# Performance work log

Measured on AMD Instinct MI355X. Metric: run time of the kernel, lower is better.

Reference implementation:

```python
import jax, jax.numpy as jnp
import numpy as np

GAMMA = 0.99
NUM_CODEWORDS = 512
CODEBOOK_DIM = 64


def setup_inputs() -> dict:
    key = jax.random.key(0)
    kx, kc = jax.random.split(key)
    x = jax.random.normal(kx, (32, 64, 64, 64), dtype=jnp.float32)  # [N,C,H,W]
    codebook = jax.random.normal(kc, (NUM_CODEWORDS, CODEBOOK_DIM), dtype=jnp.float32) / 2
    N_state = jnp.ones((NUM_CODEWORDS,), dtype=jnp.float32)
    m_state = codebook.copy()
    return {"x": x, "codebook": codebook, "N_state": N_state, "m_state": m_state}


def reference(x, codebook, N_state, m_state):
    N, C, H, W = x.shape
    K = codebook.shape[0]
    # flatten to tokens: [N*H*W, C]
    xf = jnp.transpose(x, (0, 2, 3, 1)).reshape(-1, C)
    d2 = (jnp.sum(xf * xf, axis=-1, keepdims=True)
          - 2.0 * (xf @ codebook.T)
          + jnp.sum(codebook * codebook, axis=-1)[None, :])
    index = jnp.argmin(d2, axis=1)  # [T]
    q = codebook[index].reshape(N, H, W, C).transpose(0, 3, 1, 2)  # [N,C,H,W]
    # straight-through estimator
    out = x + jax.lax.stop_gradient(q - x)
    # EMA update (training path, no_grad in original)
    counts = jax.ops.segment_sum(jnp.ones_like(index, dtype=x.dtype), index, num_segments=K)
    sums = jax.ops.segment_sum(xf, index, num_segments=K)  # [K,C]
    occupied = counts > 0
    N_new = jnp.where(occupied, N_state * GAMMA + counts * (1.0 - GAMMA), N_state)
    m_new = jnp.where(occupied[:, None], m_state * GAMMA + sums * (1.0 - GAMMA), m_state)
    codebook_new = m_new / N_new[:, None]
    return out, codebook_new, N_new, m_new
```

## Files before the change

### kernel.cpp

```cpp
#include <hip/hip_runtime.h>

static constexpr int Nn_ = 32, Cc_ = 64, Hh_ = 64, Ww_ = 64;
static constexpr int K_ = 512;
static constexpr int HW_ = Hh_ * Ww_;
static constexpr int CHW_ = Cc_ * HW_;
static constexpr int T_ = Nn_ * Hh_ * Ww_;
static constexpr int OUT_ELEMS = Nn_ * Cc_ * Hh_ * Ww_;
static constexpr int OFF_CB = OUT_ELEMS;
static constexpr int OFF_N  = OUT_ELEMS + 32768;
static constexpr int OFF_M  = OUT_ELEMS + 32768 + 512;

static constexpr int WS_IDX     = 0;
static constexpr int WS_FIXCNT  = T_;
static constexpr int WS_FIXLIST = T_ + 1;
static constexpr int WS_CBH     = 262148;
static constexpr int WS_CBL     = WS_CBH + 16384;
static constexpr int WS_CN      = WS_CBL + 16384;
static constexpr int WS_CNA     = WS_CN + 512;
static constexpr int WS_PART    = 295940;
static constexpr int SLICE_F    = K_ * Cc_ + K_;

static constexpr float THETA = 0.002f;

typedef _Float16 half8  __attribute__((ext_vector_type(8)));
typedef float    f32x16 __attribute__((ext_vector_type(16)));

__global__ __launch_bounds__(256) void k_prep(const float* __restrict__ cb,
                                              float* __restrict__ ws) {
    int j = blockIdx.x * 256 + threadIdx.x;
    if (j == 0) ((int*)(ws + WS_FIXCNT))[0] = 0;
    float v = cb[j];
    _Float16 h = (_Float16)v;
    _Float16 lo = (_Float16)(v - (float)h);
    ((_Float16*)(ws + WS_CBH))[j] = h;
    ((_Float16*)(ws + WS_CBL))[j] = lo;
    float sq = v * v;
#pragma unroll
    for (int m = 1; m < 64; m <<= 1) sq += __shfl_xor(sq, m);
    if ((threadIdx.x & 63) == 0) {
        int k = j >> 6;
        ws[WS_CN + k] = sq;
        int t = k >> 5, r5 = k & 31;
        int hi = (r5 >> 2) & 1;
        int reg = (r5 & 3) + 4 * (r5 >> 3);
        ws[WS_CNA + hi * 256 + t * 16 + reg] = sq;
    }
}

__global__ __launch_bounds__(256, 3) void k_assign(const float* __restrict__ x,
                                                   const float* __restrict__ cb,
                                                   float* __restrict__ ws,
                                                   float* __restrict__ out) {
    __shared__ alignas(16) unsigned char smem[52224];
    int* bi_s   = (int*)(smem + 51200);
    int* cert_s = (int*)(smem + 51712);

    const int b    = blockIdx.x;
    const int tid  = threadIdx.x;
    const int lane = tid & 63;
    const int wv   = tid >> 6;
    const int row0 = 2 * b, row1 = 2 * b + 1;
    const int xb0 = (row0 >> 6) * CHW_ + (row0 & 63) * Ww_;
    const int xb1 = (row1 >> 6) * CHW_ + (row1 & 63) * Ww_;

    {
        const int s  = tid & 31;
        const int c8 = tid >> 5;
        const int r  = s >> 4, wq = s & 15;
        half8 hp[4], lp[4];
#pragma unroll
        for (int stp = 0; stp < 8; ++stp) {
            int ch = c8 * 8 + stp;
            float4 v = *(const float4*)(x + (r ? xb1 : xb0) + ch * HW_ + 4 * wq);
            float vv[4] = {v.x, v.y, v.z, v.w};
#pragma unroll
            for (int j = 0; j < 4; ++j) {
                _Float16 h = (_Float16)vv[j];
                _Float16 lo = (_Float16)(vv[j] - (float)h);
                hp[j][stp] = h; lp[j][stp] = lo;
            }
        }
        const int blk = c8 ^ (wq & 7);
#pragma unroll
        for (int j = 0; j < 4; ++j) {
            int tt = 64 * r + 4 * wq + j;
            *(half8*)(smem + tt * 128 + blk * 16) = hp[j];
            *(half8*)(smem + 16384 + tt * 128 + blk * 16) = lp[j];
        }
        ((float*)(smem + 49152))[tid]       = ws[WS_CNA + tid];
        ((float*)(smem + 49152))[tid + 256] = ws[WS_CNA + tid + 256];
    }

    const char* cbh_g = (const char*)(ws + WS_CBH);
    const char* cbl_g = (const char*)(ws + WS_CBL);
    {
        float4 h4 = *(const float4*)(cbh_g + tid * 16);
        float4 l4 = *(const float4*)(cbl_g + tid * 16);
        int r = tid >> 3, p = (tid & 7) ^ (r & 7);
        *(float4*)(smem + 32768 + r * 128 + p * 16) = h4;
        *(float4*)(smem + 32768 + 4096 + r * 128 + p * 16) = l4;
    }
    __syncthreads();

    const int tb = 32 * wv + (lane & 31);
    const int hi = lane >> 5;
    half8 bh[4], bl[4];
    {
        const int tsw = (tb >> 2) & 7;
#pragma unroll
        for (int ks = 0; ks < 4; ++ks) {
            int blk = (2 * ks + hi) ^ tsw;
            bh[ks] = *(const half8*)(smem + tb * 128 + blk * 16);
            bl[ks] = *(const half8*)(smem + 16384 + tb * 128 + blk * 16);
        }
    }

    const float* cnA = (const float*)(smem + 49152);
    const int R = lane & 31;
    float bd1 = __int_as_float(0x7f800000);
    float bd2 = __int_as_float(0x7f800000);
    int bk1 = 0;

#pragma unroll 1
    for (int t = 0; t < 16; ++t) {
        const int cur = t & 1;
        float4 nh, nl;
        if (t < 15) {
            nh = *(const float4*)(cbh_g + (t + 1) * 4096 + tid * 16);
            nl = *(const float4*)(cbl_g + (t + 1) * 4096 + tid * 16);
        }
        const char* cb_b = (const char*)smem + 32768 + cur * 8192;
        half8 ah[4], al[4];
#pragma unroll
        for (int ks = 0; ks < 4; ++ks) {
            int p = (2 * ks + hi) ^ (R & 7);
            ah[ks] = *(const half8*)(cb_b + R * 128 + p * 16);
            al[ks] = *(const half8*)(cb_b + 4096 + R * 128 + p * 16);
        }
        f32x16 acc = {0.f,0.f,0.f,0.f, 0.f,0.f,0.f,0.f,
                      0.f,0.f,0.f,0.f, 0.f,0.f,0.f,0.f};
#pragma unroll
        for (int ks = 0; ks < 4; ++ks) {
            acc = __builtin_amdgcn_mfma_f32_32x32x16_f16(ah[ks], bh[ks], acc, 0, 0, 0);
            acc = __builtin_amdgcn_mfma_f32_32x32x16_f16(ah[ks], bl[ks], acc, 0, 0, 0);
            acc = __builtin_amdgcn_mfma_f32_32x32x16_f16(al[ks], bh[ks], acc, 0, 0, 0);
        }
        float cnv[16];
        {
            const float* cnp = cnA + hi * 256 + t * 16;
            *(float4*)&cnv[0]  = *(const float4*)(cnp);
            *(float4*)&cnv[4]  = *(const float4*)(cnp + 4);
            *(float4*)&cnv[8]  = *(const float4*)(cnp + 8);
            *(float4*)&cnv[12] = *(const float4*)(cnp + 12);
        }
        const int tb16 = t << 4;
#pragma unroll
        for (int j = 0; j < 16; ++j) {
            float d = fmaf(-2.0f, acc[j], cnv[j]);
            int kid = tb16 | j;
            bool lt = d < bd1;
            bd2 = lt ? bd1 : fminf(bd2, d);
            bk1 = lt ? kid : bk1;
            bd1 = fminf(bd1, d);
        }
        if (t < 15) {
            int r = tid >> 3, p2 = (tid & 7) ^ (r & 7);
            char* nb = (char*)smem + 32768 + (cur ^ 1) * 8192;
            *(float4*)(nb + r * 128 + p2 * 16) = nh;
            *(float4*)(nb + 4096 + r * 128 + p2 * 16) = nl;
        }
        __syncthreads();
    }

    {
        int t0 = bk1 >> 4, j0 = bk1 & 15;
        int rk = 32 * t0 + (j0 & 3) + 8 * (j0 >> 2) + 4 * hi;
        unsigned uf = __float_as_uint(bd1);
        uf = (uf & 0x80000000u) ? ~uf : (uf | 0x80000000u);
        unsigned long long me = ((unsigned long long)uf << 32) | (unsigned)rk;
        unsigned long long ot = (unsigned long long)__shfl_xor((long long)me, 32);
        float od1 = __shfl_xor(bd1, 32);
        float od2 = __shfl_xor(bd2, 32);
        unsigned long long m1 = (me < ot) ? me : ot;
        float d1m = fminf(bd1, od1);
        float d2m = fminf(fminf(bd2, od2), fmaxf(bd1, od1));
        if (hi == 0) {
            int k1 = (int)(m1 & 0xffffffffu);
            bool cert = (d2m - d1m) > THETA;
            bi_s[tb] = k1;
            cert_s[tb] = cert ? 1 : 0;
            ((int*)(ws + WS_IDX))[128 * b + tb] = k1;
            if (!cert) {
                int pos = atomicAdd((int*)(ws + WS_FIXCNT), 1);
                ((int*)(ws + WS_FIXLIST))[pos] = 128 * b + tb;
            }
        }
    }
    __syncthreads();

    float (*qt)[132] = (float(*)[132])smem;
#pragma unroll
    for (int jj = 0; jj < 32; ++jj) {
        int tt = wv * 32 + jj;
        qt[lane][tt] = cb[bi_s[tt] * 64 + lane];
    }
    __syncthreads();
#pragma unroll
    for (int r = 0; r < 2; ++r)
#pragma unroll
        for (int j = 0; j < 16; ++j) {
            int c = wv * 16 + j;
            out[(r ? xb1 : xb0) + c * HW_ + lane] = qt[c][64 * r + lane];
        }
}

__global__ __launch_bounds__(256) void k_fix(const float* __restrict__ x,
                                             const float* __restrict__ cb,
                                             float* __restrict__ ws,
                                             float* __restrict__ out) {
    __shared__ float xw[4][64];
    const int tid = threadIdx.x, wv = tid >> 6, lane = tid & 63;
    const int cnt = *(const int*)(ws + WS_FIXCNT);
    const int* list = (const int*)(ws + WS_FIXLIST);

    for (int it = blockIdx.x * 4 + wv; it < cnt; it += 256 * 4) {
        int g = list[it];
        int n = g >> 12, hw = g & 4095;
        const float* xp = x + n * CHW_ + hw;
        float xv = xp[lane * HW_];
        xw[wv][lane] = xv;
        unsigned long long best = ~0ull;
#pragma unroll 1
        for (int jj = 0; jj < 8; ++jj) {
            int k = lane + 64 * jj;
            const float4* cr = (const float4*)(cb + k * 64);
            float dot = 0.f;
#pragma unroll
            for (int q = 0; q < 16; ++q) {
                float4 cv = cr[q];
                dot = fmaf(cv.x, xw[wv][4 * q + 0], dot);
                dot = fmaf(cv.y, xw[wv][4 * q + 1], dot);
                dot = fmaf(cv.z, xw[wv][4 * q + 2], dot);
                dot = fmaf(cv.w, xw[wv][4 * q + 3], dot);
            }
            float d = fmaf(-2.0f, dot, ws[WS_CN + k]);
            unsigned uf = __float_as_uint(d);
            uf = (uf & 0x80000000u) ? ~uf : (uf | 0x80000000u);
            unsigned long long cd = ((unsigned long long)uf << 32) | (unsigned)k;
            if (cd < best) best = cd;
        }
#pragma unroll
        for (int m = 1; m < 64; m <<= 1) {
            unsigned long long o = (unsigned long long)__shfl_xor((long long)best, m);
            if (o < best) best = o;
        }
        int k1 = (int)(best & 0xffffffffu);
        out[n * CHW_ + lane * HW_ + hw] = cb[k1 * 64 + lane];
        if (lane == 0) ((int*)(ws + WS_IDX))[g] = k1;
    }
}

__global__ __launch_bounds__(1024, 4) void k_stats(const float* __restrict__ x,
                                                   const float* __restrict__ ws_ro,
                                                   float* __restrict__ ws,
                                                   int TPB) {
    __shared__ float xt[2][64][65];
    __shared__ float pcnt[512];
    __shared__ int   idx_s[512];

    const int tid  = threadIdx.x;
    const int bid  = blockIdx.x;
    const int wv   = tid >> 6;
    const int lane = tid & 63;
    const int hi   = lane >> 5;
    const int m    = lane & 31;
    const int NCH  = TPB >> 6;

    f32x16 acc0 = {0.f,0.f,0.f,0.f, 0.f,0.f,0.f,0.f,
                   0.f,0.f,0.f,0.f, 0.f,0.f,0.f,0.f};
    f32x16 acc1 = acc0;

    if (tid < 512) pcnt[tid] = 0.f;
    const int* __restrict__ idxg = (const int*)ws_ro;

    const int cS = tid >> 4, tq = tid & 15;
    {
        int tok0 = bid * TPB;
        int n = tok0 >> 12, hw0 = tok0 & 4095;
        float4 v = *(const float4*)(x + n * CHW_ + cS * HW_ + hw0 + 4 * tq);
        xt[0][4 * tq + 0][cS] = v.x;
        xt[0][4 * tq + 1][cS] = v.y;
        xt[0][4 * tq + 2][cS] = v.z;
        xt[0][4 * tq + 3][cS] = v.w;
    }

    int cur = 0;
    int k0 = 0;
    const int kb = (wv << 5) + m;

#pragma unroll 1
    for (int cc = 0; cc < NCH; ++cc) {
        const bool hasnext = (cc + 1 < NCH);
        float4 v;
        if (hasnext) {
            int tok0 = bid * TPB + (cc + 1) * 64;
            int n = tok0 >> 12, hw0 = tok0 & 4095;
            v = *(const float4*)(x + n * CHW_ + cS * HW_ + hw0 + 4 * tq);
        }
        if ((cc & 7) == 0 && tid < 512)
            k0 = idxg[bid * TPB + (cc >> 3) * 512 + tid];
        __syncthreads();
        if ((cc & 7) == 0) {
            if (tid < 512) { idx_s[tid] = k0; atomicAdd(&pcnt[k0], 1.0f); }
            __syncthreads();
        }

#pragma unroll
        for (int st = 0; st < 4; ++st) {
            const int t0 = st * 16 + 8 * hi;
            int ii[8];
#pragma unroll
            for (int j = 0; j < 8; ++j)
                ii[j] = idx_s[((cc & 7) << 6) + t0 + j];
            half8 bh0, bl0, bh1, bl1;
#pragma unroll
            for (int j = 0; j < 8; ++j) {
                float f0 = xt[cur][t0 + j][m];
                float f1 = xt[cur][t0 + j][32 + m];
                _Float16 h0 = (_Float16)f0;
                _Float16 h1 = (_Float16)f1;
                bh0[j] = h0; bl0[j] = (_Float16)(f0 - (float)h0);
                bh1[j] = h1; bl1[j] = (_Float16)(f1 - (float)h1);
            }
            half8 ah;
#pragma unroll
            for (int j = 0; j < 8; ++j)
                ah[j] = (ii[j] == kb) ? (_Float16)1.0f : (_Float16)0.0f;
            acc0 = __builtin_amdgcn_mfma_f32_32x32x16_f16(ah, bh0, acc0, 0, 0, 0);
            acc0 = __builtin_amdgcn_mfma_f32_32x32x16_f16(ah, bl0, acc0, 0, 0, 0);
            acc1 = __builtin_amdgcn_mfma_f32_32x32x16_f16(ah, bh1, acc1, 0, 0, 0);
            acc1 = __builtin_amdgcn_mfma_f32_32x32x16_f16(ah, bl1, acc1, 0, 0, 0);
        }

        if (hasnext) {
            xt[cur ^ 1][4 * tq + 0][cS] = v.x;
            xt[cur ^ 1][4 * tq + 1][cS] = v.y;
            xt[cur ^ 1][4 * tq + 2][cS] = v.z;
            xt[cur ^ 1][4 * tq + 3][cS] = v.w;
            cur ^= 1;
        }
    }
    __syncthreads();

    float* pb = ws + WS_PART + (size_t)bid * SLICE_F;
#pragma unroll
    for (int r = 0; r < 16; ++r) {
        int k = (wv << 5) + (r & 3) + 8 * (r >> 2) + 4 * hi;
        pb[k * 64 + m]      = acc0[r];
        pb[k * 64 + 32 + m] = acc1[r];
    }
    if (tid < 512) pb[32768 + tid] = pcnt[tid];
}

__global__ __launch_bounds__(256) void k_final(const float* __restrict__ Ns,
                                               const float* __restrict__ ms,
                                               const float* __restrict__ ws,
                                               float* __restrict__ out,
                                               int P) {
    int i = blockIdx.x * 256 + threadIdx.x;
    int k = i >> 6, c = i & 63;

    const float* base = ws + WS_PART;
    float s = 0.f, cnt = 0.f;
#pragma unroll 8
    for (int p = 0; p < P; ++p) {
        s   += base[(size_t)p * SLICE_F + i];
        cnt += base[(size_t)p * SLICE_F + 32768 + k];
    }

    const float gamma = 0.99f;
    const float omg   = (float)(1.0 - 0.99);

    bool occ = cnt > 0.0f;
    float Nv = Ns[k];
    float Nnew = occ ? (Nv * gamma + cnt * omg) : Nv;

    float mv = ms[i];
    float mnew = occ ? (mv * gamma + s * omg) : mv;

    out[OFF_CB + i] = mnew / Nnew;
    out[OFF_M  + i] = mnew;
    if (c == 0) out[OFF_N + k] = Nnew;
}

extern "C" void kernel_launch(void* const* d_in, const int* in_sizes, int n_in,
                              void* d_out, int out_size, void* d_ws, size_t ws_size,
                              hipStream_t stream) {
    const float* x  = (const float*)d_in[0];
    const float* cb = (const float*)d_in[1];
    const float* Ns = (const float*)d_in[2];
    const float* ms = (const float*)d_in[3];
    float* out = (float*)d_out;
    float* ws  = (float*)d_ws;

    int P = 256;
    while (P > 32 &&
           ((size_t)WS_PART + (size_t)P * SLICE_F) * 4 > ws_size)
        P >>= 1;
    int TPB = T_ / P;

    hipLaunchKernelGGL(k_prep,   dim3(128),  dim3(256),  0, stream, cb, ws);
    hipLaunchKernelGGL(k_assign, dim3(1024), dim3(256),  0, stream, x, cb, ws, out);
    hipLaunchKernelGGL(k_fix,    dim3(256),  dim3(256),  0, stream, x, cb, ws, out);
    hipLaunchKernelGGL(k_stats,  dim3(P),    dim3(1024), 0, stream, x, ws, ws, TPB);
    hipLaunchKernelGGL(k_final,  dim3(128),  dim3(256),  0, stream, Ns, ms, ws, out, P);
}
```

Measured before the change: 190.4 us.

## Fold codebook prep into assign, atomically reduce stats, batch fix tokens

Removes the separate codebook-prep kernel: k_assign now computes codebook norms and the fp16 hi/lo split in-kernel and cuts its shared memory so it can target 4 blocks per CU. k_stats writes its per-block partial sums with global atomics into a single accumulator, zeroed by a new small kernel, instead of 256 partial slices that k_final had to sum. k_fix now handles 8 uncertain tokens per wave, so each codebook row read serves all of them. This trades extra redundant codebook conversion work per block and atomic contention for less global traffic and fewer launches, and float atomics make the sums order-nondeterministic.

```diff
diff --git a/kernel.cpp b/kernel.cpp
--- a/kernel.cpp
+++ b/kernel.cpp
@@ -10,50 +10,29 @@
 static constexpr int OFF_N  = OUT_ELEMS + 32768;
 static constexpr int OFF_M  = OUT_ELEMS + 32768 + 512;
 
-static constexpr int WS_IDX     = 0;
-static constexpr int WS_FIXCNT  = T_;
-static constexpr int WS_FIXLIST = T_ + 1;
-static constexpr int WS_CBH     = 262148;
-static constexpr int WS_CBL     = WS_CBH + 16384;
-static constexpr int WS_CN      = WS_CBL + 16384;
-static constexpr int WS_CNA     = WS_CN + 512;
-static constexpr int WS_PART    = 295940;
-static constexpr int SLICE_F    = K_ * Cc_ + K_;
+static constexpr int WS_ACC     = 0;
+static constexpr int ACC_CNT    = 32768;
+static constexpr int WS_FIXCNT  = 33280;
+static constexpr int WS_FIXLIST = 33284;
+static constexpr int WS_IDX     = 164356;
 
 static constexpr float THETA = 0.002f;
 
 typedef _Float16 half8  __attribute__((ext_vector_type(8)));
 typedef float    f32x16 __attribute__((ext_vector_type(16)));
 
-__global__ __launch_bounds__(256) void k_prep(const float* __restrict__ cb,
-                                              float* __restrict__ ws) {
-    int j = blockIdx.x * 256 + threadIdx.x;
-    if (j == 0) ((int*)(ws + WS_FIXCNT))[0] = 0;
-    float v = cb[j];
-    _Float16 h = (_Float16)v;
-    _Float16 lo = (_Float16)(v - (float)h);
-    ((_Float16*)(ws + WS_CBH))[j] = h;
-    ((_Float16*)(ws + WS_CBL))[j] = lo;
-    float sq = v * v;
-#pragma unroll
-    for (int m = 1; m < 64; m <<= 1) sq += __shfl_xor(sq, m);
-    if ((threadIdx.x & 63) == 0) {
-        int k = j >> 6;
-        ws[WS_CN + k] = sq;
-        int t = k >> 5, r5 = k & 31;
-        int hi = (r5 >> 2) & 1;
-        int reg = (r5 & 3) + 4 * (r5 >> 3);
-        ws[WS_CNA + hi * 256 + t * 16 + reg] = sq;
-    }
-}
-
-__global__ __launch_bounds__(256, 3) void k_assign(const float* __restrict__ x,
+__global__ __launch_bounds__(256) void k_zero(float* __restrict__ ws) {
+    int i = blockIdx.x * 256 + threadIdx.x;
+    if (i < 8321) ((float4*)ws)[i] = make_float4(0.f, 0.f, 0.f, 0.f);
+}
+
+__global__ __launch_bounds__(256, 4) void k_assign(const float* __restrict__ x,
                                                    const float* __restrict__ cb,
                                                    float* __restrict__ ws,
                                                    float* __restrict__ out) {
-    __shared__ alignas(16) unsigned char smem[52224];
-    int* bi_s   = (int*)(smem + 51200);
-    int* cert_s = (int*)(smem + 51712);
+    __shared__ alignas(16) unsigned char smem[35840];
+    float* cn_s = (float*)(smem + 32768);
+    int*   bi_s = (int*)(smem + 34816);
 
     const int b    = blockIdx.x;
     const int tid  = threadIdx.x;
@@ -87,18 +66,17 @@
             *(half8*)(smem + tt * 128 + blk * 16) = hp[j];
             *(half8*)(smem + 16384 + tt * 128 + blk * 16) = lp[j];
         }
-        ((float*)(smem + 49152))[tid]       = ws[WS_CNA + tid];
-        ((float*)(smem + 49152))[tid + 256] = ws[WS_CNA + tid + 256];
-    }
-
-    const char* cbh_g = (const char*)(ws + WS_CBH);
-    const char* cbl_g = (const char*)(ws + WS_CBL);
-    {
-        float4 h4 = *(const float4*)(cbh_g + tid * 16);
-        float4 l4 = *(const float4*)(cbl_g + tid * 16);
-        int r = tid >> 3, p = (tid & 7) ^ (r & 7);
-        *(float4*)(smem + 32768 + r * 128 + p * 16) = h4;
-        *(float4*)(smem + 32768 + 4096 + r * 128 + p * 16) = l4;
+    }
+    for (int r2 = tid; r2 < 512; r2 += 256) {
+        const float4* cr = (const float4*)(cb + r2 * 64);
+        float a = 0.f;
+#pragma unroll
+        for (int i = 0; i < 16; ++i) {
+            float4 v = cr[i];
+            a = fmaf(v.x, v.x, a); a = fmaf(v.y, v.y, a);
+            a = fmaf(v.z, v.z, a); a = fmaf(v.w, v.w, a);
+        }
+        cn_s[r2] = a;
     }
     __syncthreads();
 
@@ -114,8 +92,24 @@
             bl[ks] = *(const half8*)(smem + 16384 + tb * 128 + blk * 16);
         }
     }
-
-    const float* cnA = (const float*)(smem + 49152);
+    __syncthreads();
+
+    {
+        int r = tid >> 3, g8 = tid & 7, p = g8 ^ (r & 7);
+        const float* src = cb + r * 64 + g8 * 8;
+        float4 a0 = *(const float4*)src, a1 = *(const float4*)(src + 4);
+        float vv[8] = {a0.x, a0.y, a0.z, a0.w, a1.x, a1.y, a1.z, a1.w};
+        half8 hh, ll;
+#pragma unroll
+        for (int j = 0; j < 8; ++j) {
+            _Float16 h = (_Float16)vv[j];
+            hh[j] = h; ll[j] = (_Float16)(vv[j] - (float)h);
+        }
+        *(half8*)(smem + 16384 + r * 128 + p * 16) = hh;
+        *(half8*)(smem + 16384 + 4096 + r * 128 + p * 16) = ll;
+    }
+    __syncthreads();
+
     const int R = lane & 31;
     float bd1 = __int_as_float(0x7f800000);
     float bd2 = __int_as_float(0x7f800000);
@@ -124,18 +118,18 @@
 #pragma unroll 1
     for (int t = 0; t < 16; ++t) {
         const int cur = t & 1;
-        float4 nh, nl;
+        float4 p0, p1;
         if (t < 15) {
-            nh = *(const float4*)(cbh_g + (t + 1) * 4096 + tid * 16);
-            nl = *(const float4*)(cbl_g + (t + 1) * 4096 + tid * 16);
-        }
-        const char* cb_b = (const char*)smem + 32768 + cur * 8192;
+            const float* src = cb + ((t + 1) * 32 + (tid >> 3)) * 64 + (tid & 7) * 8;
+            p0 = *(const float4*)src; p1 = *(const float4*)(src + 4);
+        }
+        const char* cb_b = (const char*)smem + 16384 + cur * 8192;
         half8 ah[4], al[4];
 #pragma unroll
         for (int ks = 0; ks < 4; ++ks) {
-            int p = (2 * ks + hi) ^ (R & 7);
-            ah[ks] = *(const half8*)(cb_b + R * 128 + p * 16);
-            al[ks] = *(const half8*)(cb_b + 4096 + R * 128 + p * 16);
+            int pI = (2 * ks + hi) ^ (R & 7);
+            ah[ks] = *(const half8*)(cb_b + R * 128 + pI * 16);
+            al[ks] = *(const half8*)(cb_b + 4096 + R * 128 + pI * 16);
         }
         f32x16 acc = {0.f,0.f,0.f,0.f, 0.f,0.f,0.f,0.f,
                       0.f,0.f,0.f,0.f, 0.f,0.f,0.f,0.f};
@@ -145,18 +139,12 @@
             acc = __builtin_amdgcn_mfma_f32_32x32x16_f16(ah[ks], bl[ks], acc, 0, 0, 0);
             acc = __builtin_amdgcn_mfma_f32_32x32x16_f16(al[ks], bh[ks], acc, 0, 0, 0);
         }
-        float cnv[16];
-        {
-            const float* cnp = cnA + hi * 256 + t * 16;
-            *(float4*)&cnv[0]  = *(const float4*)(cnp);
-            *(float4*)&cnv[4]  = *(const float4*)(cnp + 4);
-            *(float4*)&cnv[8]  = *(const float4*)(cnp + 8);
-            *(float4*)&cnv[12] = *(const float4*)(cnp + 12);
-        }
+        const int kt0 = t * 32 + 4 * hi;
         const int tb16 = t << 4;
 #pragma unroll
         for (int j = 0; j < 16; ++j) {
-            float d = fmaf(-2.0f, acc[j], cnv[j]);
+            float cn = cn_s[kt0 + (j & 3) + 8 * (j >> 2)];
+            float d = fmaf(-2.0f, acc[j], cn);
             int kid = tb16 | j;
             bool lt = d < bd1;
             bd2 = lt ? bd1 : fminf(bd2, d);
@@ -164,10 +152,17 @@
             bd1 = fminf(bd1, d);
         }
         if (t < 15) {
-            int r = tid >> 3, p2 = (tid & 7) ^ (r & 7);
-            char* nb = (char*)smem + 32768 + (cur ^ 1) * 8192;
-            *(float4*)(nb + r * 128 + p2 * 16) = nh;
-            *(float4*)(nb + 4096 + r * 128 + p2 * 16) = nl;
+            int r = tid >> 3, g8 = tid & 7, p = g8 ^ (r & 7);
+            float vv[8] = {p0.x, p0.y, p0.z, p0.w, p1.x, p1.y, p1.z, p1.w};
+            half8 hh, ll;
+#pragma unroll
+            for (int j = 0; j < 8; ++j) {
+                _Float16 h = (_Float16)vv[j];
+                hh[j] = h; ll[j] = (_Float16)(vv[j] - (float)h);
+            }
+            char* nb = (char*)smem + 16384 + (cur ^ 1) * 8192;
+            *(half8*)(nb + r * 128 + p * 16) = hh;
+            *(half8*)(nb + 4096 + r * 128 + p * 16) = ll;
         }
         __syncthreads();
     }
@@ -186,11 +181,9 @@
         float d2m = fminf(fminf(bd2, od2), fmaxf(bd1, od1));
         if (hi == 0) {
             int k1 = (int)(m1 & 0xffffffffu);
-            bool cert = (d2m - d1m) > THETA;
             bi_s[tb] = k1;
-            cert_s[tb] = cert ? 1 : 0;
             ((int*)(ws + WS_IDX))[128 * b + tb] = k1;
-            if (!cert) {
+            if (!((d2m - d1m) > THETA)) {
                 int pos = atomicAdd((int*)(ws + WS_FIXCNT), 1);
                 ((int*)(ws + WS_FIXLIST))[pos] = 128 * b + tb;
             }
@@ -198,7 +191,7 @@
     }
     __syncthreads();
 
-    float (*qt)[132] = (float(*)[132])smem;
+    float (*qt)[131] = (float(*)[131])smem;
 #pragma unroll
     for (int jj = 0; jj < 32; ++jj) {
         int tt = wv * 32 + jj;
@@ -218,45 +211,73 @@
                                              const float* __restrict__ cb,
                                              float* __restrict__ ws,
                                              float* __restrict__ out) {
-    __shared__ float xw[4][64];
+    __shared__ float xw[4][8][64];
     const int tid = threadIdx.x, wv = tid >> 6, lane = tid & 63;
     const int cnt = *(const int*)(ws + WS_FIXCNT);
     const int* list = (const int*)(ws + WS_FIXLIST);
-
-    for (int it = blockIdx.x * 4 + wv; it < cnt; it += 256 * 4) {
-        int g = list[it];
-        int n = g >> 12, hw = g & 4095;
-        const float* xp = x + n * CHW_ + hw;
-        float xv = xp[lane * HW_];
-        xw[wv][lane] = xv;
-        unsigned long long best = ~0ull;
+    int* idxg = (int*)(ws + WS_IDX);
+
+    for (int base = (blockIdx.x * 4 + wv) * 8; base < cnt; base += 256 * 4 * 8) {
+        const int nt = min(8, cnt - base);
+        int gg[8];
+#pragma unroll
+        for (int j = 0; j < 8; ++j) {
+            gg[j] = 0;
+            if (j < nt) {
+                int g = list[base + j]; gg[j] = g;
+                int n = g >> 12, hw = g & 4095;
+                xw[wv][j][lane] = x[n * CHW_ + lane * HW_ + hw];
+            }
+        }
+        unsigned long long best[8];
+#pragma unroll
+        for (int j = 0; j < 8; ++j) best[j] = ~0ull;
+
 #pragma unroll 1
         for (int jj = 0; jj < 8; ++jj) {
-            int k = lane + 64 * jj;
+            const int k = lane + 64 * jj;
             const float4* cr = (const float4*)(cb + k * 64);
-            float dot = 0.f;
+            float cn = 0.f;
+            float dt[8] = {0.f,0.f,0.f,0.f,0.f,0.f,0.f,0.f};
 #pragma unroll
             for (int q = 0; q < 16; ++q) {
                 float4 cv = cr[q];
-                dot = fmaf(cv.x, xw[wv][4 * q + 0], dot);
-                dot = fmaf(cv.y, xw[wv][4 * q + 1], dot);
-                dot = fmaf(cv.z, xw[wv][4 * q + 2], dot);
-                dot = fmaf(cv.w, xw[wv][4 * q + 3], dot);
-            }
-            float d = fmaf(-2.0f, dot, ws[WS_CN + k]);
-            unsigned uf = __float_as_uint(d);
-            uf = (uf & 0x80000000u) ? ~uf : (uf | 0x80000000u);
-            unsigned long long cd = ((unsigned long long)uf << 32) | (unsigned)k;
-            if (cd < best) best = cd;
-        }
-#pragma unroll
-        for (int m = 1; m < 64; m <<= 1) {
-            unsigned long long o = (unsigned long long)__shfl_xor((long long)best, m);
-            if (o < best) best = o;
-        }
-        int k1 = (int)(best & 0xffffffffu);
-        out[n * CHW_ + lane * HW_ + hw] = cb[k1 * 64 + lane];
-        if (lane == 0) ((int*)(ws + WS_IDX))[g] = k1;
+                cn = fmaf(cv.x, cv.x, cn); cn = fmaf(cv.y, cv.y, cn);
+                cn = fmaf(cv.z, cv.z, cn); cn = fmaf(cv.w, cv.w, cn);
+#pragma unroll
+                for (int j = 0; j < 8; ++j) {
+                    float4 xv = *(const float4*)&xw[wv][j][4 * q];
+                    dt[j] = fmaf(cv.x, xv.x, dt[j]);
+                    dt[j] = fmaf(cv.y, xv.y, dt[j]);
+                    dt[j] = fmaf(cv.z, xv.z, dt[j]);
+                    dt[j] = fmaf(cv.w, xv.w, dt[j]);
+                }
+            }
+#pragma unroll
+            for (int j = 0; j < 8; ++j) {
+                float d = fmaf(-2.0f, dt[j], cn);
+                unsigned uf = __float_as_uint(d);
+                uf = (uf & 0x80000000u) ? ~uf : (uf | 0x80000000u);
+                unsigned long long cd = ((unsigned long long)uf << 32) | (unsigned)k;
+                if (cd < best[j]) best[j] = cd;
+            }
+        }
+#pragma unroll
+        for (int j = 0; j < 8; ++j) {
+            if (j < nt) {
+                unsigned long long b2 = best[j];
+#pragma unroll
+                for (int m = 1; m < 64; m <<= 1) {
+                    unsigned long long o = (unsigned long long)__shfl_xor((long long)b2, m);
+                    if (o < b2) b2 = o;
+                }
+                int k1 = (int)(b2 & 0xffffffffu);
+                int g = gg[j];
+                int n = g >> 12, hw = g & 4095;
+                out[n * CHW_ + lane * HW_ + hw] = cb[k1 * 64 + lane];
+                if (lane == 0) idxg[g] = k1;
+            }
+        }
     }
 }
 
@@ -281,7 +302,7 @@
     f32x16 acc1 = acc0;
 
     if (tid < 512) pcnt[tid] = 0.f;
-    const int* __restrict__ idxg = (const int*)ws_ro;
+    const int* __restrict__ idxg = (const int*)(ws_ro + WS_IDX);
 
     const int cS = tid >> 4, tq = tid & 15;
     {
@@ -352,31 +373,29 @@
     }
     __syncthreads();
 
-    float* pb = ws + WS_PART + (size_t)bid * SLICE_F;
+    float* acc_g = ws + WS_ACC;
 #pragma unroll
     for (int r = 0; r < 16; ++r) {
         int k = (wv << 5) + (r & 3) + 8 * (r >> 2) + 4 * hi;
-        pb[k * 64 + m]      = acc0[r];
-        pb[k * 64 + 32 + m] = acc1[r];
-    }
-    if (tid < 512) pb[32768 + tid] = pcnt[tid];
+        if (pcnt[k] > 0.f) {
+            atomicAdd(acc_g + k * 64 + m,      acc0[r]);
+            atomicAdd(acc_g + k * 64 + 32 + m, acc1[r]);
+        }
+    }
+    if (tid < 512 && pcnt[tid] > 0.f)
+        atomicAdd(acc_g + ACC_CNT + tid, pcnt[tid]);
 }
 
 __global__ __launch_bounds__(256) void k_final(const float* __restrict__ Ns,
                                                const float* __restrict__ ms,
                                                const float* __restrict__ ws,
-                                               float* __restrict__ out,
-                                               int P) {
+                                               float* __restrict__ out) {
     int i = blockIdx.x * 256 + threadIdx.x;
     int k = i >> 6, c = i & 63;
 
-    const float* base = ws + WS_PART;
-    float s = 0.f, cnt = 0.f;
-#pragma unroll 8
-    for (int p = 0; p < P; ++p) {
-        s   += base[(size_t)p * SLICE_F + i];
-        cnt += base[(size_t)p * SLICE_F + 32768 + k];
-    }
+    const float* acc = ws + WS_ACC;
+    float s   = acc[i];
+    float cnt = acc[ACC_CNT + k];
 
     const float gamma = 0.99f;
     const float omg   = (float)(1.0 - 0.99);
@@ -403,15 +422,9 @@
     float* out = (float*)d_out;
     float* ws  = (float*)d_ws;
 
-    int P = 256;
-    while (P > 32 &&
-           ((size_t)WS_PART + (size_t)P * SLICE_F) * 4 > ws_size)
-        P >>= 1;
-    int TPB = T_ / P;
-
-    hipLaunchKernelGGL(k_prep,   dim3(128),  dim3(256),  0, stream, cb, ws);
+    hipLaunchKernelGGL(k_zero,   dim3(33),   dim3(256),  0, stream, ws);
     hipLaunchKernelGGL(k_assign, dim3(1024), dim3(256),  0, stream, x, cb, ws, out);
     hipLaunchKernelGGL(k_fix,    dim3(256),  dim3(256),  0, stream, x, cb, ws, out);
-    hipLaunchKernelGGL(k_stats,  dim3(P),    dim3(1024), 0, stream, x, ws, ws, TPB);
-    hipLaunchKernelGGL(k_final,  dim3(128),  dim3(256),  0, stream, Ns, ms, ws, out, P);
-}
+    hipLaunchKernelGGL(k_stats,  dim3(256),  dim3(1024), 0, stream, x, ws, ws, 512);
+    hipLaunchKernelGGL(k_final,  dim3(128),  dim3(256),  0, stream, Ns, ms, ws, out);
+}
```

After: 245.1 us. 28.7% more time.
